# Kernel optimization log

Measured on AMD Instinct MI355X. Metric: run time of the kernel, lower is better.

Reference implementation:

```python
import jax, jax.numpy as jnp
import numpy as np

B, N, C, K, T = 64, 1024, 256, 512, 64
D_THRESH = 0.5
POWER_ITERS = 20


def _pdist(x):
    # x: [..., K, 3] -> pairwise euclidean distances [..., K, K]
    n = jnp.sum(x * x, axis=-1)
    sq = n[..., :, None] + n[..., None, :] - 2.0 * jnp.einsum('...kc,...lc->...kl', x, x)
    return jnp.sqrt(jnp.maximum(sq, 0.0) + 1e-12)


def _forward(rt, rt_centroids, rt_cls_attn, shift_and_scale, W_in, b_in, W1, b1, W2, b2,
             num_rt, anc_idx, pos_idx, neg_idx):
    valid = jnp.arange(N)[None, :] < num_rt[:, None]                      # [B,N]
    # Normalize.batch_unnormalize: pts * scale + shift on valid tokens
    shift = shift_and_scale[:, None, :3]
    scale = shift_and_scale[:, None, 3:4]
    cent = jnp.where(valid[..., None], rt_centroids * scale + shift, rt_centroids)
    attn = jnp.where(valid, rt_cls_attn, -1e9)
    _, top_idx = jax.lax.top_k(attn, K)                                   # [B,K]
    cent_k = jnp.take_along_axis(cent, top_idx[..., None], axis=1)        # [B,K,3]
    rt_k = jnp.take_along_axis(rt, top_idx[..., None], axis=1)            # [B,K,C]
    # SGV padding mask [T,2,K,K]: rows masked by anchor count, cols by pos/neg counts
    n_eff = jnp.minimum(num_rt, K)
    r = jnp.arange(K)
    row_mask = r[None, :] < n_eff[anc_idx][:, None]                       # [T,K]
    col_mask = jnp.stack([r[None, :] < n_eff[pos_idx][:, None],
                          r[None, :] < n_eff[neg_idx][:, None]], axis=1)  # [T,2,K]
    mask = row_mask[:, None, :, None] & col_mask[:, :, None, :]           # [T,2,K,K]
    # input_linear on anchor / neighbour relay tokens
    anc_f = rt_k[anc_idx] @ W_in + b_in                                   # [T,K,C]
    nn_f = jnp.stack([rt_k[pos_idx], rt_k[neg_idx]], axis=1) @ W_in + b_in  # [T,2,K,C]
    anc_c = cent_k[anc_idx]                                               # [T,K,3]
    nn_c = jnp.stack([cent_k[pos_idx], cent_k[neg_idx]], axis=1)          # [T,2,K,3]
    # feature-space nearest-neighbour correspondences anc -> nn (SpectralGV style)
    fd = (jnp.sum(anc_f ** 2, -1)[:, None, :, None]
          + jnp.sum(nn_f ** 2, -1)[:, :, None, :]
          - 2.0 * jnp.einsum('tkc,tnlc->tnkl', anc_f, nn_f))              # [T,2,K,K]
    corr = jnp.argmin(fd, axis=-1)                                        # [T,2,K]
    q_c = jnp.take_along_axis(nn_c, corr[..., None], axis=2)              # [T,2,K,3]
    q_f = jnp.take_along_axis(nn_f, corr[..., None], axis=2)              # [T,2,K,C]
    # correspondence confidence from feature cosine similarity
    cos = jnp.sum(anc_f[:, None] * q_f, -1) / (
        jnp.linalg.norm(anc_f, axis=-1)[:, None] * jnp.linalg.norm(q_f, axis=-1) + 1e-8)
    s = jax.nn.relu(cos)                                                  # [T,2,K]
    # threshold-masked geometric consistency adjacency
    d_p = _pdist(anc_c)[:, None]                                          # [T,1,K,K]
    d_q = _pdist(q_c)                                                     # [T,2,K,K]
    geo = (jnp.abs(d_p - d_q) < D_THRESH) & mask & (~jnp.eye(K, dtype=bool))
    A = geo.astype(jnp.float32) * s[..., :, None] * s[..., None, :]       # [T,2,K,K]
    # leading eigenvector via power iteration (A is entrywise nonnegative)
    v = jnp.full((T, 2, K), 1.0 / np.sqrt(K), dtype=jnp.float32)
    for _ in range(POWER_ITERS):
        w = jnp.einsum('tnkl,tnl->tnk', A, v)
        v = w / (jnp.linalg.norm(w, axis=-1, keepdims=True) + 1e-8)
    eig = -jnp.sort(-v, axis=-1)                                          # sort_eigvec, descending
    h = jax.nn.relu(eig @ W1 + b1)
    scores = jax.nn.sigmoid(h @ W2 + b2)                                  # [T,2,1]
    targets = jnp.zeros_like(scores).at[:, 0].set(1.0)
    return scores, targets


def setup_inputs() -> dict:
    key = jax.random.key(0)
    ks = jax.random.split(key, 12)
    return {
        'rt': jax.random.normal(ks[0], (B, N, C), jnp.float32),
        'rt_centroids': jax.random.normal(ks[1], (B, N, 3), jnp.float32),
        'rt_cls_attn': jax.random.uniform(ks[2], (B, N), jnp.float32),
        'shift_and_scale': jax.random.uniform(ks[3], (B, 4), jnp.float32),
        'num_rt': jax.random.randint(ks[4], (B,), 128, N, jnp.int32),
        'anc_idx': jax.random.randint(ks[5], (T,), 0, B, jnp.int32),
        'pos_idx': jax.random.randint(ks[6], (T,), 0, B, jnp.int32),
        'neg_idx': jax.random.randint(ks[7], (T,), 0, B, jnp.int32),
        'W_in': jax.random.normal(ks[8], (C, C), jnp.float32) / np.sqrt(C),
        'b_in': jnp.zeros((C,), jnp.float32),
        'W1': jax.random.normal(ks[9], (K, K), jnp.float32) / np.sqrt(K),
        'b1': jnp.zeros((K,), jnp.float32),
        'W2': jax.random.normal(ks[10], (K, 1), jnp.float32) / np.sqrt(K),
        'b2': jnp.zeros((1,), jnp.float32),
    }


def reference(rt, rt_centroids, rt_cls_attn, shift_and_scale, num_rt, anc_idx, pos_idx, neg_idx,
              W_in, b_in, W1, b1, W2, b2):
    return _forward(rt, rt_centroids, rt_cls_attn, shift_and_scale, W_in, b_in, W1, b1, W2, b2,
                    num_rt, anc_idx, pos_idx, neg_idx)
```

## Files before the change

kernel.cpp:

```cpp
#include <hip/hip_runtime.h>
#include <cstddef>

#define BB 64
#define NN 1024
#define CC 256
#define KK 512
#define TT 64
#define NPAIR 128

typedef _Float16 h8 __attribute__((ext_vector_type(8)));
typedef _Float16 h4 __attribute__((ext_vector_type(4)));
typedef float f4 __attribute__((ext_vector_type(4)));

typedef __attribute__((address_space(1))) const void GV;
typedef __attribute__((address_space(3))) void LV;
#define GLDS16(g, s) __builtin_amdgcn_global_load_lds((GV*)(const void*)(g), (LV*)(void*)(s), 16, 0, 0)


__global__ __launch_bounds__(256) void wtrans_kernel(
    const float* __restrict__ Win, _Float16* __restrict__ wth, _Float16* __restrict__ wtl)
{
    __shared__ float t[64][65];
    const int k0 = blockIdx.x * 64, n0 = blockIdx.y * 64;
    const int tid = threadIdx.x;
    const int c = tid & 63, r0 = tid >> 6;
    for (int r = r0; r < 64; r += 4)
        t[r][c] = Win[(size_t)(k0 + r) * CC + n0 + c];
    __syncthreads();
    for (int r = r0; r < 64; r += 4) {
        float x = t[c][r];
        _Float16 h = (_Float16)x;
        size_t o = (size_t)(n0 + r) * CC + k0 + c;
        wth[o] = h;
        wtl[o] = (_Float16)(x - (float)h);
    }
}

__global__ __launch_bounds__(512) void sel_kernel(
    const float* __restrict__ attn, const float* __restrict__ cents,
    const float* __restrict__ sas, const int* __restrict__ num_rt,
    int* __restrict__ topidx, int* __restrict__ neff, float* __restrict__ centk)
{
    __shared__ unsigned long long keys[1024];
    const int b = blockIdx.x, tid = threadIdx.x;
    const int nr = num_rt[b];
    for (int i = tid; i < 1024; i += 512) {
        float a = (i < nr) ? attn[b * NN + i] : -1e9f;
        unsigned u = __float_as_uint(a);
        u = (u & 0x80000000u) ? ~u : (u | 0x80000000u);
        keys[i] = ((unsigned long long)u << 32) | (unsigned)(0xFFFFFFFFu - (unsigned)i);
    }
    __syncthreads();
    for (int k = 2; k <= 1024; k <<= 1) {
        for (int j = k >> 1; j > 0; j >>= 1) {
            int i = ((tid & ~(j - 1)) << 1) | (tid & (j - 1));
            int p = i | j;
            unsigned long long a = keys[i], c = keys[p];
            bool up = (i & k) == 0;
            if (up ? (a < c) : (a > c)) { keys[i] = c; keys[p] = a; }
            __syncthreads();
        }
    }
    {
        unsigned long long key = keys[tid];
        int idx = (int)(~(unsigned)key);
        float x = cents[(b * NN + idx) * 3 + 0];
        float y = cents[(b * NN + idx) * 3 + 1];
        float z = cents[(b * NN + idx) * 3 + 2];
        if (idx < nr) {
            float sc = sas[b * 4 + 3];
            x = x * sc + sas[b * 4 + 0];
            y = y * sc + sas[b * 4 + 1];
            z = z * sc + sas[b * 4 + 2];
        }
        float nc = x * x + y * y + z * z;
        ((float4*)centk)[b * KK + tid] = make_float4(x, y, z, nc);
        topidx[b * KK + tid] = idx;
    }
    if (tid == 0) neff[b] = (nr < KK) ? nr : KK;
}

__global__ __launch_bounds__(256) void feat_mfma(
    const float* __restrict__ rt, const int* __restrict__ topidx,
    const _Float16* __restrict__ wth, const _Float16* __restrict__ wtl,
    const float* __restrict__ bin,
    _Float16* __restrict__ feath, _Float16* __restrict__ featl)
{
    const int mtile = blockIdx.x, nt = blockIdx.y;
    __shared__ _Float16 Ah[128][32], Al[128][32], Bh[128][32], Bl[128][32];
    __shared__ int tix[128];
    const int tid = threadIdx.x;
    const int w = tid >> 6, lane = tid & 63;
    const int quad = lane >> 4, l16 = lane & 15;
    const int wm = (w >> 1) * 64, wl = (w & 1) * 64;
    const int b = mtile >> 2;
    if (tid < 128) tix[tid] = topidx[mtile * 128 + tid];
    __syncthreads();
    const int arow_i = tid >> 1;
    const int aseg = (tid & 1) * 16;
    const float* arow = rt + ((size_t)b * NN + tix[arow_i]) * CC + aseg;
    _Float16* bsh = (w < 2) ? &Bh[0][0] : &Bl[0][0];
    const _Float16* bplane = (w < 2) ? wth : wtl;
    const int rowi = lane >> 2, chunk = lane & 3;

    f4 acc[4][4];
    #pragma unroll
    for (int i = 0; i < 4; i++)
        #pragma unroll
        for (int j = 0; j < 4; j++)
            acc[i][j] = (f4){0.f, 0.f, 0.f, 0.f};

    for (int k0 = 0; k0 < CC; k0 += 32) {
        __syncthreads();
        #pragma unroll
        for (int jj = 0; jj < 4; jj++) {
            int j = (w & 1) * 4 + jj;
            int row = j * 16 + rowi;
            GLDS16(bplane + (size_t)(nt * 128 + row) * CC + k0 + chunk * 8, bsh + j * 512);
        }
        {
            const float4* src = (const float4*)(arow + k0);
            #pragma unroll
            for (int c = 0; c < 2; c++) {
                float4 p = src[2 * c], q2 = src[2 * c + 1];
                float xv[8] = {p.x, p.y, p.z, p.w, q2.x, q2.y, q2.z, q2.w};
                h8 hv, lv;
                #pragma unroll
                for (int j = 0; j < 8; j++) {
                    _Float16 h = (_Float16)xv[j];
                    hv[j] = h;
                    lv[j] = (_Float16)(xv[j] - (float)h);
                }
                *(h8*)&Ah[arow_i][aseg + c * 8] = hv;
                *(h8*)&Al[arow_i][aseg + c * 8] = lv;
            }
        }
        __syncthreads();
        h8 afh[4], afl[4], bfh[4], bfl[4];
        #pragma unroll
        for (int i = 0; i < 4; i++) {
            int ra = wm + i * 16 + l16;
            int rb = wl + i * 16 + l16;
            afh[i] = *(const h8*)&Ah[ra][quad * 8];
            afl[i] = *(const h8*)&Al[ra][quad * 8];
            bfh[i] = *(const h8*)&Bh[rb][quad * 8];
            bfl[i] = *(const h8*)&Bl[rb][quad * 8];
        }
        #pragma unroll
        for (int i = 0; i < 4; i++)
            #pragma unroll
            for (int j = 0; j < 4; j++) {
                acc[i][j] = __builtin_amdgcn_mfma_f32_16x16x32_f16(afh[i], bfh[j], acc[i][j], 0, 0, 0);
                acc[i][j] = __builtin_amdgcn_mfma_f32_16x16x32_f16(afh[i], bfl[j], acc[i][j], 0, 0, 0);
                acc[i][j] = __builtin_amdgcn_mfma_f32_16x16x32_f16(afl[i], bfh[j], acc[i][j], 0, 0, 0);
            }
    }
    #pragma unroll
    for (int j = 0; j < 4; j++) {
        int col = wl + j * 16 + l16;
        float bj = bin[nt * 128 + col];
        #pragma unroll
        for (int i = 0; i < 4; i++)
            #pragma unroll
            for (int r = 0; r < 4; r++) {
                int row = wm + i * 16 + quad * 4 + r;
                float v = acc[i][j][r] + bj;
                _Float16 h = (_Float16)v;
                size_t o = (size_t)(mtile * 128 + row) * CC + nt * 128 + col;
                feath[o] = h;
                featl[o] = (_Float16)(v - (float)h);
            }
    }
}

__global__ __launch_bounds__(256) void norm_kernel(
    const _Float16* __restrict__ feath, const _Float16* __restrict__ featl,
    float* __restrict__ normF)
{
    int r = blockIdx.x * 4 + (threadIdx.x >> 6);
    int lane = threadIdx.x & 63;
    h4 hv = ((const h4*)(feath + (size_t)r * CC))[lane];
    h4 lv = ((const h4*)(featl + (size_t)r * CC))[lane];
    float s = 0.f;
    #pragma unroll
    for (int j = 0; j < 4; j++) {
        float x = (float)hv[j] + (float)lv[j];
        s += x * x;
    }
    for (int off = 32; off; off >>= 1) s += __shfl_down(s, off);
    if (lane == 0) normF[r] = s;
}

__global__ __launch_bounds__(512) void argmin_mfma(
    const _Float16* __restrict__ feath, const _Float16* __restrict__ featl,
    const float* __restrict__ normF,
    const int* __restrict__ anc, const int* __restrict__ pos, const int* __restrict__ neg,
    float* __restrict__ partv, int* __restrict__ partl, float* __restrict__ partd)
{
    const int id = blockIdx.x;
    const int xcd = id & 7, kgrp = id >> 3;
    const int pr = xcd * 16 + (kgrp >> 2);
    const int s = kgrp & 3;
    const int lt = s & 1, kt = s >> 1;
    const int t = pr >> 1, nn2 = pr & 1;
    const int a = anc[t];
    const int bb = nn2 ? neg[t] : pos[t];
    const size_t Abase = ((size_t)a * KK + kt * 256) * CC;
    const size_t Bbase = ((size_t)bb * KK + lt * 256) * CC;
    __shared__ _Float16 S[2][4][8192];
    __shared__ float rdv[256][2];
    __shared__ int   rdl[256][2];
    __shared__ float rdd[256][2];
    const int tid = threadIdx.x;
    const int w = tid >> 6, lane = tid & 63;
    const int quad = lane >> 4, l16 = lane & 15;
    const int wr = w >> 1, wc = w & 1;
    const int rowi = lane >> 2, chunk = lane & 3;
    const int plane = w >> 1;
    const int srow = (w & 1) * 128;
    const _Float16* gsrc = (plane == 0) ? feath + Abase
                         : (plane == 1) ? featl + Abase
                         : (plane == 2) ? feath + Bbase
                         :                featl + Bbase;
    const _Float16* grow = gsrc + (size_t)(srow + rowi) * CC + chunk * 8;

    f4 acc[4][8];
    #pragma unroll
    for (int i = 0; i < 4; i++)
        #pragma unroll
        for (int j = 0; j < 8; j++)
            acc[i][j] = (f4){0.f, 0.f, 0.f, 0.f};

    #pragma unroll
    for (int j = 0; j < 8; j++)
        GLDS16(grow + (size_t)(j * 16) * CC, &S[0][plane][srow * 32 + j * 512]);

    #pragma unroll
    for (int kk = 0; kk < 8; kk++) {
        const int cb = kk & 1;
        if (kk < 7) {
            const int k1 = (kk + 1) * 32;
            #pragma unroll
            for (int j = 0; j < 8; j++)
                GLDS16(grow + (size_t)(j * 16) * CC + k1, &S[cb ^ 1][plane][srow * 32 + j * 512]);
            asm volatile("s_waitcnt vmcnt(8)" ::: "memory");
        } else {
            asm volatile("s_waitcnt vmcnt(0)" ::: "memory");
        }
        __builtin_amdgcn_s_barrier();
        h8 afh[4], afl[4];
        #pragma unroll
        for (int i = 0; i < 4; i++) {
            int ra = wr * 64 + i * 16 + l16;
            afh[i] = *(const h8*)&S[cb][0][ra * 32 + quad * 8];
            afl[i] = *(const h8*)&S[cb][1][ra * 32 + quad * 8];
        }
        #pragma unroll
        for (int j = 0; j < 8; j++) {
            int rb = wc * 128 + j * 16 + l16;
            h8 bfh = *(const h8*)&S[cb][2][rb * 32 + quad * 8];
            h8 bfl = *(const h8*)&S[cb][3][rb * 32 + quad * 8];
            #pragma unroll
            for (int i = 0; i < 4; i++) {
                acc[i][j] = __builtin_amdgcn_mfma_f32_16x16x32_f16(afh[i], bfh, acc[i][j], 0, 0, 0);
                acc[i][j] = __builtin_amdgcn_mfma_f32_16x16x32_f16(afh[i], bfl, acc[i][j], 0, 0, 0);
                acc[i][j] = __builtin_amdgcn_mfma_f32_16x16x32_f16(afl[i], bfh, acc[i][j], 0, 0, 0);
            }
        }
        __builtin_amdgcn_sched_barrier(0);
        __builtin_amdgcn_s_barrier();
    }
    float nbj[8];
    #pragma unroll
    for (int j = 0; j < 8; j++)
        nbj[j] = normF[(size_t)bb * KK + lt * 256 + wc * 128 + j * 16 + l16];
    #pragma unroll
    for (int i = 0; i < 4; i++) {
        #pragma unroll
        for (int r = 0; r < 4; r++) {
            float bv = INFINITY; int bl = 0; float bd = 0.f;
            #pragma unroll
            for (int j = 0; j < 8; j++) {
                float d = acc[i][j][r];
                float v = nbj[j] - 2.f * d;
                int l = lt * 256 + wc * 128 + j * 16 + l16;
                if (v < bv) { bv = v; bl = l; bd = d; }
            }
            #pragma unroll
            for (int off = 1; off < 16; off <<= 1) {
                float ov = __shfl_xor(bv, off);
                int   ol = __shfl_xor(bl, off);
                float od = __shfl_xor(bd, off);
                if (ov < bv || (ov == bv && ol < bl)) { bv = ov; bl = ol; bd = od; }
            }
            if (l16 == 0) {
                int row = wr * 64 + i * 16 + quad * 4 + r;
                rdv[row][wc] = bv;
                rdl[row][wc] = bl;
                rdd[row][wc] = bd;
            }
        }
    }
    __syncthreads();
    if (tid < 256) {
        float bv = rdv[tid][0]; int bl = rdl[tid][0]; float bd = rdd[tid][0];
        float v1 = rdv[tid][1]; int l1 = rdl[tid][1];
        if (v1 < bv || (v1 == bv && l1 < bl)) { bv = v1; bl = l1; bd = rdd[tid][1]; }
        size_t idx = ((size_t)pr * KK + kt * 256 + tid) * 2 + lt;
        partv[idx] = bv; partl[idx] = bl; partd[idx] = bd;
    }
}

__global__ __launch_bounds__(256) void geo_kernel(
    const float* __restrict__ centk,
    const float* __restrict__ partv, const int* __restrict__ partl,
    const float* __restrict__ partd, const float* __restrict__ normF,
    const int* __restrict__ neff,
    const int* __restrict__ anc, const int* __restrict__ pos, const int* __restrict__ neg,
    float* __restrict__ sbuf, unsigned* __restrict__ gmask)
{
    const int kt = blockIdx.x;
    const int lt4 = blockIdx.y;
    const int pair = blockIdx.z;
    const int t = pair >> 1, nn2 = pair & 1;
    const int a = anc[t];
    const int bb2 = (nn2 == 0) ? pos[t] : neg[t];
    const int nea = neff[a], neb = neff[bb2];
    const bool writer = (kt == 0) && (lt4 == 0);
    __shared__ int ci[512];
    __shared__ __align__(16) float4 ca[512], cq[512];
    for (int i = threadIdx.x; i < KK; i += 256) {
        size_t base = ((size_t)pair * KK + i) * 2;
        float bv = partv[base]; int bl = partl[base]; float bd = partd[base];
        float v = partv[base + 1]; int l = partl[base + 1];
        if (v < bv || (v == bv && l < bl)) { bv = v; bl = l; bd = partd[base + 1]; }
        ci[i] = bl;
        if (writer) {
            float na = normF[(size_t)a * KK + i];
            float nb = normF[(size_t)bb2 * KK + bl];
            float cosv = bd / (sqrtf(na) * sqrtf(nb) + 1e-8f);
            sbuf[pair * KK + i] = fmaxf(cosv, 0.f);
        }
    }
    __syncthreads();
    for (int i = threadIdx.x; i < KK; i += 256) {
        ca[i] = ((const float4*)centk)[a * KK + i];
        cq[i] = ((const float4*)centk)[bb2 * KK + ci[i]];
    }
    __syncthreads();
    const int k = kt * 256 + threadIdx.x;
    float4 pk = ca[k], qk = cq[k];
    bool rowm = k < nea;
    unsigned* outp = gmask + ((size_t)pair * KK + k) * 16 + lt4 * 4;
    for (int w = 0; w < 4; w++) {
        unsigned word = 0;
        #pragma unroll
        for (int bi = 0; bi < 32; bi++) {
            int l = lt4 * 128 + w * 32 + bi;
            float4 pl = ca[l], ql = cq[l];
            float dp2 = pk.w + pl.w - 2.f * (pk.x * pl.x + pk.y * pl.y + pk.z * pl.z);
            float dp = sqrtf(fmaxf(dp2, 0.f) + 1e-12f);
            float dq2 = qk.w + ql.w - 2.f * (qk.x * ql.x + qk.y * ql.y + qk.z * ql.z);
            float dq = sqrtf(fmaxf(dq2, 0.f) + 1e-12f);
            bool g = (fabsf(dp - dq) < 0.5f) && rowm && (l < neb) && (l != k);
            word |= (g ? (1u << bi) : 0u);
        }
        outp[w] = word;
    }
}

__global__ __launch_bounds__(1024, 4) void power_kernel(
    const unsigned* __restrict__ gmask, const float* __restrict__ sbuf,
    const int* __restrict__ neff,
    const int* __restrict__ anc, const int* __restrict__ pos, const int* __restrict__ neg,
    const float* __restrict__ W1, const float* __restrict__ b1,
    const float* __restrict__ W2, const float* __restrict__ b2,
    float* __restrict__ out)
{
    const int pair = blockIdx.x;
    const int tid = threadIdx.x;
    const int row = tid & 511;
    const int half = tid >> 9;
    const int tt = pair >> 1, nn2 = pair & 1;
    const int a = anc[tt];
    const int bb2 = (nn2 == 0) ? pos[tt] : neg[tt];
    const int nea = neff[a], neb = neff[bb2];
    __shared__ __align__(16) float uu[512];
    __shared__ float T[64][257];
    __shared__ float pacc[1024];
    __shared__ float red[16];
    __shared__ float ev[512];
    __shared__ float hpart[1024];
    __shared__ int convflag;
    unsigned m[8];
    const unsigned* g = gmask + ((size_t)pair * KK + row) * 16 + half * 8;
    #pragma unroll
    for (int w = 0; w < 8; w++) m[w] = g[w];
    const float s = sbuf[pair * KK + row];
    const int wbase = tid & 511 & ~63;
    const bool wact = (wbase < nea);
    int nw = (neb - half * 256 + 31) >> 5;
    nw = (nw < 0) ? 0 : (nw > 8 ? 8 : nw);
    const int bp = tid & 63;
    const int vh = tid >> 6;
    #define UADDR(r) ((((r) & 4) << 6) + (((r) >> 3) << 2) + ((r) & 3))
    const int GV_[16] = {0,1,3,2,6,7,5,4,12,13,15,14,10,11,9,8};
    const int GB[15] = {0,1,0,2,0,1,0,3,0,1,0,2,0,1,0};
    const float GS[15] = {1.f,1.f,-1.f,1.f,1.f,-1.f,-1.f,1.f,1.f,1.f,-1.f,-1.f,1.f,-1.f,-1.f};
    float v = 0.044194173824159216f;
    float vnprev = v;
    if (half == 0) uu[UADDR(row)] = s * v;
    __syncthreads();
    for (int it = 0; it < 20; it++) {
        {
            float4 ulo = *(const float4*)&uu[bp * 4];
            float4 uhi = *(const float4*)&uu[256 + bp * 4];
            float ul[4] = {ulo.x, ulo.y, ulo.z, ulo.w};
            float H = 0.f;
            H += (float)((vh >> 0) & 1) * uhi.x;
            H += (float)((vh >> 1) & 1) * uhi.y;
            H += (float)((vh >> 2) & 1) * uhi.z;
            H += (float)((vh >> 3) & 1) * uhi.w;
            float L = 0.f;
            T[bp][vh * 16 + 0] = H;
            #pragma unroll
            for (int k = 1; k < 16; k++) {
                L += GS[k - 1] * ul[GB[k - 1]];
                T[bp][vh * 16 + GV_[k]] = H + L;
            }
        }
        __syncthreads();
        float a0 = 0.f, a1 = 0.f, a2 = 0.f, a3 = 0.f;
        if (wact) {
            #define GATHERW(w)  do { unsigned mw = m[w]; \
                const int p0 = half * 32 + (w) * 4; \
                a0 += T[p0 + 0][mw & 255u]; \
                a1 += T[p0 + 1][(mw >> 8) & 255u]; \
                a2 += T[p0 + 2][(mw >> 16) & 255u]; \
                a3 += T[p0 + 3][mw >> 24]; } while (0)
            if (nw > 0) GATHERW(0);
            if (nw > 1) GATHERW(1);
            if (nw > 2) GATHERW(2);
            if (nw > 3) GATHERW(3);
            if (nw > 4) GATHERW(4);
            if (nw > 5) GATHERW(5);
            if (nw > 6) GATHERW(6);
            if (nw > 7) GATHERW(7);
            #undef GATHERW
        }
        pacc[tid] = (a0 + a1) + (a2 + a3);
        __syncthreads();
        float wk = s * (pacc[row] + pacc[row + 512]);
        if ((it & 3) == 3) {
            float t2 = wk * wk;
            for (int off = 32; off; off >>= 1) t2 += __shfl_down(t2, off);
            if ((tid & 63) == 0) red[tid >> 6] = t2;
            if (tid == 0) convflag = 1;
            __syncthreads();
            float tot = 0.f;
            #pragma unroll
            for (int x = 0; x < 16; x++) tot += red[x];
            tot *= 0.5f;
            v = wk / (sqrtf(tot) + 1e-8f);
            bool eq = (__float_as_uint(v) == __float_as_uint(vnprev));
            vnprev = v;
            if (half == 0) uu[UADDR(row)] = s * v;
            if (!eq) convflag = 0;
            __syncthreads();
            if (convflag) break;
        } else {
            if (half == 0) uu[UADDR(row)] = s * wk;
            __syncthreads();
        }
    }
    if (half == 0) ev[row] = v;
    __syncthreads();
    for (int kk = 2; kk <= 512; kk <<= 1) {
        for (int j = kk >> 1; j; j >>= 1) {
            if (tid < 256) {
                int i = ((tid & ~(j - 1)) << 1) | (tid & (j - 1));
                int p = i | j;
                float x = ev[i], y = ev[p];
                bool up = (i & kk) == 0;
                if (up ? (x < y) : (x > y)) { ev[i] = y; ev[p] = x; }
            }
            __syncthreads();
        }
    }
    const int cbase = half * 256;
    float h = (half == 0) ? b1[row] : 0.f;
    #pragma unroll 8
    for (int l = 0; l < 256; l++)
        h += ev[cbase + l] * W1[(size_t)(cbase + l) * KK + row];
    hpart[tid] = h;
    __syncthreads();
    float term = 0.f;
    if (half == 0) {
        float hv = fmaxf(hpart[row] + hpart[row + 512], 0.f);
        term = hv * W2[row];
    }
    for (int off = 32; off; off >>= 1) term += __shfl_down(term, off);
    if ((tid & 63) == 0) red[tid >> 6] = term;
    __syncthreads();
    if (tid == 0) {
        float sc = 0.f;
        #pragma unroll
        for (int x = 0; x < 16; x++) sc += red[x];
        sc += b2[0];
        out[pair] = 1.f / (1.f + expf(-sc));
        out[NPAIR + pair] = (pair & 1) ? 0.f : 1.f;
    }
}

extern "C" void kernel_launch(void* const* d_in, const int* in_sizes, int n_in,
                              void* d_out, int out_size, void* d_ws, size_t ws_size,
                              hipStream_t stream) {
    (void)in_sizes; (void)n_in; (void)out_size; (void)ws_size;
    const float* rt    = (const float*)d_in[0];
    const float* cents = (const float*)d_in[1];
    const float* attn  = (const float*)d_in[2];
    const float* sas   = (const float*)d_in[3];
    const int* num_rt  = (const int*)d_in[4];
    const int* anc     = (const int*)d_in[5];
    const int* pos     = (const int*)d_in[6];
    const int* neg     = (const int*)d_in[7];
    const float* Win   = (const float*)d_in[8];
    const float* bin   = (const float*)d_in[9];
    const float* W1    = (const float*)d_in[10];
    const float* b1    = (const float*)d_in[11];
    const float* W2    = (const float*)d_in[12];
    const float* b2    = (const float*)d_in[13];

    float* ws = (float*)d_ws;
    _Float16* feath = (_Float16*)ws;
    _Float16* featl = (_Float16*)(ws + 4194304);
    float* normF = ws + 8388608;
    float* centk = ws + 8421376;
    float* sbuf  = ws + 8552448;
    int* topidx  = (int*)(ws + 8617984);
    int* neffp   = (int*)(ws + 8650752);
    unsigned* gmask = (unsigned*)(ws + 8716352);
    _Float16* wth = (_Float16*)(ws + 8716352 + 786432);
    _Float16* wtl = (_Float16*)(ws + 8716352 + 819200);
    float* partv = (float*)(ws + 9764928);
    int*   partl = (int*)(ws + 10027072);
    float* partd = (float*)(ws + 10289216);
    float* out = (float*)d_out;

    wtrans_kernel<<<dim3(4, 4), 256, 0, stream>>>(Win, wth, wtl);
    sel_kernel<<<64, 512, 0, stream>>>(attn, cents, sas, num_rt, topidx, neffp, centk);
    feat_mfma<<<dim3(256, 2), 256, 0, stream>>>(rt, topidx, wth, wtl, bin, feath, featl);
    norm_kernel<<<8192, 256, 0, stream>>>(feath, featl, normF);
    argmin_mfma<<<512, 512, 0, stream>>>(feath, featl, normF, anc, pos, neg, partv, partl, partd);
    geo_kernel<<<dim3(2, 4, 128), 256, 0, stream>>>(centk, partv, partl, partd, normF, neffp, anc, pos, neg, sbuf, gmask);
    power_kernel<<<128, 1024, 0, stream>>>(gmask, sbuf, neffp, anc, pos, neg, W1, b1, W2, b2, out);
}
```

Baseline: 342.1 us.

## Fuse row-norm into feature GEMM epilogue and split power-iteration tail into separate kernel

Row squared norms are now accumulated in the feat_mfma epilogue, reduced by shuffles and shared memory, and added atomically into a zeroed normF, so the separate norm_kernel and its re-read of the features disappear. The power kernel now writes eigenvector values to global memory, and a new tail_kernel does the sort and MLP, which frees shared memory in power_kernel. The change adds a memset and an extra launch. The norm is now taken from the fp32 value before the hi/lo split, and atomic accumulation order may vary slightly between runs.

```diff
diff --git a/kernel.cpp b/kernel.cpp
--- a/kernel.cpp
+++ b/kernel.cpp
@@ -84,11 +84,13 @@
     const float* __restrict__ rt, const int* __restrict__ topidx,
     const _Float16* __restrict__ wth, const _Float16* __restrict__ wtl,
     const float* __restrict__ bin,
-    _Float16* __restrict__ feath, _Float16* __restrict__ featl)
+    _Float16* __restrict__ feath, _Float16* __restrict__ featl,
+    float* __restrict__ normF)
 {
     const int mtile = blockIdx.x, nt = blockIdx.y;
     __shared__ _Float16 Ah[128][32], Al[128][32], Bh[128][32], Bl[128][32];
     __shared__ int tix[128];
+    __shared__ float rowpart[128][2];
     const int tid = threadIdx.x;
     const int w = tid >> 6, lane = tid & 63;
     const int quad = lane >> 4, l16 = lane & 15;
@@ -155,6 +157,12 @@
                 acc[i][j] = __builtin_amdgcn_mfma_f32_16x16x32_f16(afl[i], bfh[j], acc[i][j], 0, 0, 0);
             }
     }
+    float rowsq[4][4];
+    #pragma unroll
+    for (int i = 0; i < 4; i++)
+        #pragma unroll
+        for (int r = 0; r < 4; r++)
+            rowsq[i][r] = 0.f;
     #pragma unroll
     for (int j = 0; j < 4; j++) {
         int col = wl + j * 16 + l16;
@@ -165,30 +173,29 @@
             for (int r = 0; r < 4; r++) {
                 int row = wm + i * 16 + quad * 4 + r;
                 float v = acc[i][j][r] + bj;
+                rowsq[i][r] += v * v;
                 _Float16 h = (_Float16)v;
                 size_t o = (size_t)(mtile * 128 + row) * CC + nt * 128 + col;
                 feath[o] = h;
                 featl[o] = (_Float16)(v - (float)h);
             }
     }
-}
-
-__global__ __launch_bounds__(256) void norm_kernel(
-    const _Float16* __restrict__ feath, const _Float16* __restrict__ featl,
-    float* __restrict__ normF)
-{
-    int r = blockIdx.x * 4 + (threadIdx.x >> 6);
-    int lane = threadIdx.x & 63;
-    h4 hv = ((const h4*)(feath + (size_t)r * CC))[lane];
-    h4 lv = ((const h4*)(featl + (size_t)r * CC))[lane];
-    float s = 0.f;
-    #pragma unroll
-    for (int j = 0; j < 4; j++) {
-        float x = (float)hv[j] + (float)lv[j];
-        s += x * x;
-    }
-    for (int off = 32; off; off >>= 1) s += __shfl_down(s, off);
-    if (lane == 0) normF[r] = s;
+    #pragma unroll
+    for (int i = 0; i < 4; i++)
+        #pragma unroll
+        for (int r = 0; r < 4; r++) {
+            float p = rowsq[i][r];
+            #pragma unroll
+            for (int off = 1; off < 16; off <<= 1)
+                p += __shfl_xor(p, off);
+            if (l16 == 0)
+                rowpart[wm + i * 16 + quad * 4 + r][w & 1] = p;
+        }
+    __syncthreads();
+    if (tid < 128) {
+        float nf = rowpart[tid][0] + rowpart[tid][1];
+        atomicAdd(normF + mtile * 128 + tid, nf);
+    }
 }
 
 __global__ __launch_bounds__(512) void argmin_mfma(
@@ -373,9 +380,7 @@
     const unsigned* __restrict__ gmask, const float* __restrict__ sbuf,
     const int* __restrict__ neff,
     const int* __restrict__ anc, const int* __restrict__ pos, const int* __restrict__ neg,
-    const float* __restrict__ W1, const float* __restrict__ b1,
-    const float* __restrict__ W2, const float* __restrict__ b2,
-    float* __restrict__ out)
+    float* __restrict__ evg)
 {
     const int pair = blockIdx.x;
     const int tid = threadIdx.x;
@@ -389,8 +394,6 @@
     __shared__ float T[64][257];
     __shared__ float pacc[1024];
     __shared__ float red[16];
-    __shared__ float ev[512];
-    __shared__ float hpart[1024];
     __shared__ int convflag;
     unsigned m[8];
     const unsigned* g = gmask + ((size_t)pair * KK + row) * 16 + half * 8;
@@ -473,7 +476,23 @@
             __syncthreads();
         }
     }
-    if (half == 0) ev[row] = v;
+    if (half == 0) evg[(size_t)pair * KK + row] = v;
+}
+
+__global__ __launch_bounds__(1024, 4) void tail_kernel(
+    const float* __restrict__ evg,
+    const float* __restrict__ W1, const float* __restrict__ b1,
+    const float* __restrict__ W2, const float* __restrict__ b2,
+    float* __restrict__ out)
+{
+    const int pair = blockIdx.x;
+    const int tid = threadIdx.x;
+    const int row = tid & 511;
+    const int half = tid >> 9;
+    __shared__ float red[16];
+    __shared__ float ev[512];
+    __shared__ float hpart[1024];
+    if (half == 0) ev[row] = evg[(size_t)pair * KK + row];
     __syncthreads();
     for (int kk = 2; kk <= 512; kk <<= 1) {
         for (int j = kk >> 1; j; j >>= 1) {
@@ -545,13 +564,15 @@
     float* partv = (float*)(ws + 9764928);
     int*   partl = (int*)(ws + 10027072);
     float* partd = (float*)(ws + 10289216);
+    float* evg   = (float*)(ws + 9764928);
     float* out = (float*)d_out;
 
+    hipMemsetAsync(normF, 0, 32768 * sizeof(float), stream);
     wtrans_kernel<<<dim3(4, 4), 256, 0, stream>>>(Win, wth, wtl);
     sel_kernel<<<64, 512, 0, stream>>>(attn, cents, sas, num_rt, topidx, neffp, centk);
-    feat_mfma<<<dim3(256, 2), 256, 0, stream>>>(rt, topidx, wth, wtl, bin, feath, featl);
-    norm_kernel<<<8192, 256, 0, stream>>>(feath, featl, normF);
+    feat_mfma<<<dim3(256, 2), 256, 0, stream>>>(rt, topidx, wth, wtl, bin, feath, featl, normF);
     argmin_mfma<<<512, 512, 0, stream>>>(feath, featl, normF, anc, pos, neg, partv, partl, partd);
     geo_kernel<<<dim3(2, 4, 128), 256, 0, stream>>>(centk, partv, partl, partd, normF, neffp, anc, pos, neg, sbuf, gmask);
-    power_kernel<<<128, 1024, 0, stream>>>(gmask, sbuf, neffp, anc, pos, neg, W1, b1, W2, b2, out);
-}
+    power_kernel<<<128, 1024, 0, stream>>>(gmask, sbuf, neffp, anc, pos, neg, evg);
+    tail_kernel<<<128, 1024, 0, stream>>>(evg, W1, b1, W2, b2, out);
+}
```

Measured after the change: 355.5 us. +3.9%, slower.
